# Kernel optimization log

Hardware: AMD Instinct MI355X
Metric: run time of the kernel (lower is better)

The kernel has to match this reference:

```python
import jax, jax.numpy as jnp
import numpy as np

N, C, K2 = 40000, 128, 9  # active voxels, channels, 3x3 kernel taps
HEAD_OUT = {"hm": 3, "center": 2, "center_z": 1, "dim": 3, "rot": 2}
EPS = 1e-5
INIT_BIAS = -2.66


def setup_inputs() -> dict:
    key = jax.random.key(0)
    ks = jax.random.split(key, 16)
    feats = jax.random.normal(ks[0], (N, C), dtype=jnp.float32)
    # precomputed submanifold-conv neighbor indices (one per kernel tap, all valid)
    nbr_idx = jax.random.randint(ks[1], (N, K2), 0, N, dtype=jnp.int32)
    H = len(HEAD_OUT)
    inp = {"feats": feats, "nbr_idx": nbr_idx}
    # stacked 3x3 SubMConv weights for all heads (kaiming-ish scale)
    inp["W1"] = jax.random.normal(ks[2], (H, K2, C, C), dtype=jnp.float32) * (2.0 / (K2 * C)) ** 0.5
    inp["gamma"] = jnp.ones((H, C), jnp.float32)
    inp["beta"] = jnp.zeros((H, C), jnp.float32)
    for i, (name, oc) in enumerate(HEAD_OUT.items()):
        inp[f"w_{name}"] = jax.random.normal(ks[3 + i], (C, oc), dtype=jnp.float32) * (2.0 / C) ** 0.5
        inp[f"b_{name}"] = (jnp.full((oc,), INIT_BIAS, jnp.float32) if name == "hm"
                             else jnp.zeros((oc,), jnp.float32))
    return inp


def reference(feats, nbr_idx, W1, gamma, beta,
              w_hm, b_hm, w_center, b_center, w_center_z, b_center_z,
              w_dim, b_dim, w_rot, b_rot):
    # SubMConv2d as gather + contraction over kernel taps (shared by all heads)
    gathered = feats[nbr_idx]                       # [N, K2, C]
    y = jnp.einsum('nkc,hkcd->hnd', gathered, W1)   # [H, N, C]
    # BatchNorm1d (training-mode forward: biased batch stats over voxels) + ReLU
    mean = y.mean(axis=1, keepdims=True)
    var = y.var(axis=1, keepdims=True)
    y = jax.nn.relu((y - mean) * jax.lax.rsqrt(var + EPS) * gamma[:, None, :] + beta[:, None, :])
    # per-head 1x1 SubMConv with bias
    heads = [(w_hm, b_hm), (w_center, b_center), (w_center_z, b_center_z),
             (w_dim, b_dim), (w_rot, b_rot)]
    outs = [y[i] @ w + b for i, (w, b) in enumerate(heads)]
    # concat head outputs along channel: [N, 3+2+1+3+2] = [N, 11]
    return jnp.concatenate(outs, axis=-1)
```

## Files before the change

kernel.cpp:

```cpp
#include <hip/hip_runtime.h>
#include <stdint.h>

#define NVOX 40000
#define CCH  128
#define K2   9
#define NH   5

typedef __attribute__((ext_vector_type(8))) short bf16x8;
typedef __attribute__((ext_vector_type(4))) float f32x4;

__device__ __forceinline__ unsigned short f2b(float f) {
  union { float f; unsigned int u; } v; v.f = f;
  return (unsigned short)((v.u + 0x7fffu + ((v.u >> 16) & 1u)) >> 16);
}
__device__ __forceinline__ float b2f(unsigned short u) {
  union { unsigned int u; float f; } v; v.u = ((unsigned int)u) << 16;
  return v.f;
}
__device__ __forceinline__ void g2l16(const void* g, void* l) {
  __builtin_amdgcn_global_load_lds(
      (const __attribute__((address_space(1))) unsigned int*)g,
      (__attribute__((address_space(3))) unsigned int*)l, 16, 0, 0);
}
__device__ __forceinline__ int swz(int row, int col) {
  return row * 128 + ((((col >> 3) ^ (row & 15)) << 3) | (col & 7));
}

__global__ void cvt_feats(const float4* __restrict__ in, ushort4* __restrict__ o, int n4) {
  int i = blockIdx.x * 256 + threadIdx.x;
  if (i < n4) {
    float4 v = in[i];
    ushort4 r;
    r.x = f2b(v.x); r.y = f2b(v.y); r.z = f2b(v.z); r.w = f2b(v.w);
    o[i] = r;
  }
}

__global__ void cvt_w1(const float* __restrict__ w1, unsigned short* __restrict__ w1t) {
  __shared__ unsigned short t[128 * 34];
  int tile = blockIdx.x;
  int q = blockIdx.y;
  const float* src = w1 + (size_t)tile * 16384 + q * 32 * 128;
  for (int e = threadIdx.x; e < 4096; e += 256) {
    int c = e >> 7, d = e & 127;
    t[d * 34 + c] = f2b(src[e]);
  }
  __syncthreads();
  unsigned short* dst = w1t + (size_t)tile * 16384 + q * 32;
  for (int e = threadIdx.x; e < 4096; e += 256) {
    int d = e >> 5, c = e & 31;
    dst[d * 128 + c] = t[d * 34 + c];
  }
}

__global__ void __launch_bounds__(256, 2) conv_gemm(
    const unsigned short* __restrict__ fb,
    const int* __restrict__ nbr,
    const unsigned short* __restrict__ w1t,
    unsigned short* __restrict__ yb,
    float* __restrict__ sums)
{
  __shared__ unsigned short As[128 * 128];
  __shared__ unsigned short Bs[128 * 128];
  __shared__ int idxs[128 * K2];

  const int h = blockIdx.y;
  const int n0 = blockIdx.x * 128;
  const int tid = threadIdx.x;
  const int wave = tid >> 6;
  const int lane = tid & 63;
  const int lrow = lane >> 4;
  const int lcol = lane & 15;
  const int wm = wave >> 1, wn = wave & 1;

  for (int i = tid; i < 128 * K2; i += 256) {
    int r = i / K2;
    int kk = i - r * K2;
    int gn = n0 + r; if (gn > NVOX - 1) gn = NVOX - 1;
    idxs[i] = nbr[gn * K2 + kk];
  }
  __syncthreads();

  f32x4 acc[4][4] = {};

  for (int k = 0; k < K2; ++k) {
    const unsigned short* wp = w1t + (((size_t)h * K2 + k) << 14);
#pragma unroll
    for (int i = 0; i < 8; ++i) {
      int elem = wave * 4096 + i * 512;
      int row = (elem >> 7) + lrow;
      g2l16(wp + row * 128 + ((lcol ^ (row & 15)) << 3), &Bs[elem]);
    }
    int ridx[8];
#pragma unroll
    for (int i = 0; i < 8; ++i)
      ridx[i] = idxs[(wave * 32 + i * 4 + lrow) * K2 + k];
#pragma unroll
    for (int i = 0; i < 8; ++i) {
      int row = wave * 32 + i * 4 + lrow;
      g2l16(fb + (size_t)ridx[i] * CCH + ((lcol ^ (row & 15)) << 3),
            &As[(wave * 32 + i * 4) * CCH]);
    }

    __syncthreads();
#pragma unroll
    for (int kc = 0; kc < 4; ++kc) {
      bf16x8 af[4], bfr[4];
#pragma unroll
      for (int mi = 0; mi < 4; ++mi) {
        int row = wm * 64 + mi * 16 + lcol;
        af[mi] = *(const bf16x8*)&As[row * CCH + (((kc * 4 + lrow) ^ (row & 15)) << 3)];
      }
#pragma unroll
      for (int ni = 0; ni < 4; ++ni) {
        int row = wn * 64 + ni * 16 + lcol;
        bfr[ni] = *(const bf16x8*)&Bs[row * CCH + (((kc * 4 + lrow) ^ (row & 15)) << 3)];
      }
#pragma unroll
      for (int mi = 0; mi < 4; ++mi)
#pragma unroll
        for (int ni = 0; ni < 4; ++ni)
          acc[mi][ni] = __builtin_amdgcn_mfma_f32_16x16x32_bf16(af[mi], bfr[ni], acc[mi][ni], 0, 0, 0);
    }
    __syncthreads();
  }

#pragma unroll
  for (int mi = 0; mi < 4; ++mi)
#pragma unroll
    for (int ni = 0; ni < 4; ++ni)
#pragma unroll
      for (int r = 0; r < 4; ++r) {
        int row = wm * 64 + mi * 16 + lrow * 4 + r;
        int col = wn * 64 + ni * 16 + lcol;
        As[swz(row, col)] = f2b(acc[mi][ni][r]);
      }
  __syncthreads();

  for (int i = tid; i < 2048; i += 256) {
    int row = i >> 4;
    int c = i & 15;
    if (n0 + row < NVOX)
      *(bf16x8*)(yb + ((size_t)h * NVOX + n0 + row) * CCH + c * 8) =
          *(const bf16x8*)&As[row * 128 + ((c ^ (row & 15)) << 3)];
  }

  {
    int col = tid & 127, half = tid >> 7;
    int rbase = half * 64;
    int nvalid = NVOX - n0 - rbase;
    if (nvalid > 64) nvalid = 64;
    float s = 0.f, q = 0.f;
    for (int r = 0; r < nvalid; ++r) {
      float z = b2f(As[swz(rbase + r, col)]);
      s += z; q += z * z;
    }
    if (nvalid > 0) {
      atomicAdd(&sums[h * CCH + col], s);
      atomicAdd(&sums[NH * CCH + h * CCH + col], q);
    }
  }
}

__global__ void finalize_bn(const float* __restrict__ sums, const float* __restrict__ gamma,
                            const float* __restrict__ beta, float* __restrict__ ssb) {
  int h = blockIdx.x, c = threadIdx.x;
  float mean = sums[h * CCH + c] * (1.f / NVOX);
  float var = sums[NH * CCH + h * CCH + c] * (1.f / NVOX) - mean * mean;
  float rstd = rsqrtf(var + 1e-5f);
  float scale = rstd * gamma[h * CCH + c];
  ssb[h * CCH + c] = scale;
  ssb[NH * CCH + h * CCH + c] = beta[h * CCH + c] - mean * scale;
}

__global__ void __launch_bounds__(256) head_fuse(
    const unsigned short* __restrict__ yb, const float* __restrict__ ssb,
    const float* __restrict__ w_hm, const float* __restrict__ b_hm,
    const float* __restrict__ w_ce, const float* __restrict__ b_ce,
    const float* __restrict__ w_cz, const float* __restrict__ b_cz,
    const float* __restrict__ w_dm, const float* __restrict__ b_dm,
    const float* __restrict__ w_rt, const float* __restrict__ b_rt,
    float* __restrict__ out)
{
  int v = blockIdx.x * 256 + threadIdx.x;
  if (v >= NVOX) return;
  float a0 = b_hm[0], a1 = b_hm[1], a2 = b_hm[2];
  float a3 = b_ce[0], a4 = b_ce[1];
  float a5 = b_cz[0];
  float a6 = b_dm[0], a7 = b_dm[1], a8 = b_dm[2];
  float a9 = b_rt[0], a10 = b_rt[1];

#define DO_HEAD(HI, BODY)                                                    \
  {                                                                          \
    const bf16x8* yp = (const bf16x8*)(yb + ((size_t)(HI)*NVOX + v) * CCH);  \
    const float* sc = ssb + (HI)*CCH;                                        \
    const float* sh = ssb + NH * CCH + (HI)*CCH;                             \
    for (int q8 = 0; q8 < 16; ++q8) {                                        \
      bf16x8 pk = yp[q8];                                                    \
      _Pragma("unroll") for (int e = 0; e < 8; ++e) {                        \
        int d = q8 * 8 + e;                                                  \
        float z = fmaf(b2f((unsigned short)pk[e]), sc[d], sh[d]);            \
        z = fmaxf(z, 0.f);                                                   \
        BODY;                                                                \
      }                                                                      \
    }                                                                        \
  }

  DO_HEAD(0, { a0 = fmaf(z, w_hm[d*3+0], a0); a1 = fmaf(z, w_hm[d*3+1], a1); a2 = fmaf(z, w_hm[d*3+2], a2); })
  DO_HEAD(1, { a3 = fmaf(z, w_ce[d*2+0], a3); a4 = fmaf(z, w_ce[d*2+1], a4); })
  DO_HEAD(2, { a5 = fmaf(z, w_cz[d], a5); })
  DO_HEAD(3, { a6 = fmaf(z, w_dm[d*3+0], a6); a7 = fmaf(z, w_dm[d*3+1], a7); a8 = fmaf(z, w_dm[d*3+2], a8); })
  DO_HEAD(4, { a9 = fmaf(z, w_rt[d*2+0], a9); a10 = fmaf(z, w_rt[d*2+1], a10); })
#undef DO_HEAD

  float* op = out + (size_t)v * 11;
  op[0] = a0; op[1] = a1; op[2] = a2; op[3] = a3; op[4] = a4; op[5] = a5;
  op[6] = a6; op[7] = a7; op[8] = a8; op[9] = a9; op[10] = a10;
}

extern "C" void kernel_launch(void* const* d_in, const int* in_sizes, int n_in,
                              void* d_out, int out_size, void* d_ws, size_t ws_size,
                              hipStream_t stream) {
  const float* feats = (const float*)d_in[0];
  const int*   nbr   = (const int*)d_in[1];
  const float* W1    = (const float*)d_in[2];
  const float* gamma = (const float*)d_in[3];
  const float* beta  = (const float*)d_in[4];
  const float* w_hm = (const float*)d_in[5];  const float* b_hm = (const float*)d_in[6];
  const float* w_ce = (const float*)d_in[7];  const float* b_ce = (const float*)d_in[8];
  const float* w_cz = (const float*)d_in[9];  const float* b_cz = (const float*)d_in[10];
  const float* w_dm = (const float*)d_in[11]; const float* b_dm = (const float*)d_in[12];
  const float* w_rt = (const float*)d_in[13]; const float* b_rt = (const float*)d_in[14];
  float* out = (float*)d_out;

  char* ws = (char*)d_ws;
  unsigned short* w1t = (unsigned short*)ws;
  unsigned short* fb  = (unsigned short*)(ws + 11796480);
  unsigned short* yb  = (unsigned short*)(ws + 22036480);
  float* sums = (float*)(ws + 73236480);
  float* ssb  = (float*)(ws + 73241600);

  hipMemsetAsync(sums, 0, 2 * NH * CCH * sizeof(float), stream);
  cvt_feats<<<5000, 256, 0, stream>>>((const float4*)feats, (ushort4*)fb, NVOX * CCH / 4);
  cvt_w1<<<dim3(45, 4), 256, 0, stream>>>(W1, w1t);
  conv_gemm<<<dim3(313, NH), 256, 0, stream>>>(fb, nbr, w1t, yb, sums);
  finalize_bn<<<NH, CCH, 0, stream>>>(sums, gamma, beta, ssb);
  head_fuse<<<157, 256, 0, stream>>>(yb, ssb, w_hm, b_hm, w_ce, b_ce, w_cz, b_cz,
                                     w_dm, b_dm, w_rt, b_rt, out);
}
```

Measured before the change: 244.2 us.

## Read conv weights from global, prefetch gathers, regroup blocks, split head kernel

The conv GEMM no longer stages weights in LDS. Each wave reads its B fragments directly from global memory, which frees LDS and lets occupancy rise to 3 blocks per SM. The next tap's feature gather is issued after the MFMA loop, and blocks are reordered so the 5 heads of each group of 8 tiles run close together to share gathered rows in cache. The two conversion kernels are merged into one launch, and the head kernel now uses one thread per (head, voxel) for more parallelism. The risk is that uncached global B loads and the single-buffered As add latency and can stall the MFMAs.

```diff
diff --git a/kernel.cpp b/kernel.cpp
--- a/kernel.cpp
+++ b/kernel.cpp
@@ -5,6 +5,7 @@
 #define CCH  128
 #define K2   9
 #define NH   5
+#define TILES 313
 
 typedef __attribute__((ext_vector_type(8))) short bf16x8;
 typedef __attribute__((ext_vector_type(4))) float f32x4;
@@ -26,20 +27,23 @@
   return row * 128 + ((((col >> 3) ^ (row & 15)) << 3) | (col & 7));
 }
 
-__global__ void cvt_feats(const float4* __restrict__ in, ushort4* __restrict__ o, int n4) {
-  int i = blockIdx.x * 256 + threadIdx.x;
-  if (i < n4) {
-    float4 v = in[i];
-    ushort4 r;
-    r.x = f2b(v.x); r.y = f2b(v.y); r.z = f2b(v.z); r.w = f2b(v.w);
-    o[i] = r;
-  }
-}
-
-__global__ void cvt_w1(const float* __restrict__ w1, unsigned short* __restrict__ w1t) {
+__global__ void prep(const float4* __restrict__ feats, ushort4* __restrict__ fb,
+                     const float* __restrict__ w1, unsigned short* __restrict__ w1t) {
   __shared__ unsigned short t[128 * 34];
-  int tile = blockIdx.x;
-  int q = blockIdx.y;
+  int b = blockIdx.x;
+  if (b < 5000) {
+    int i = b * 256 + threadIdx.x;
+    if (i < NVOX * CCH / 4) {
+      float4 v = feats[i];
+      ushort4 r;
+      r.x = f2b(v.x); r.y = f2b(v.y); r.z = f2b(v.z); r.w = f2b(v.w);
+      fb[i] = r;
+    }
+    return;
+  }
+  int bb = b - 5000;
+  int tile = bb >> 2;
+  int q = bb & 3;
   const float* src = w1 + (size_t)tile * 16384 + q * 32 * 128;
   for (int e = threadIdx.x; e < 4096; e += 256) {
     int c = e >> 7, d = e & 127;
@@ -53,7 +57,7 @@
   }
 }
 
-__global__ void __launch_bounds__(256, 2) conv_gemm(
+__global__ void __launch_bounds__(256, 3) conv_gemm(
     const unsigned short* __restrict__ fb,
     const int* __restrict__ nbr,
     const unsigned short* __restrict__ w1t,
@@ -61,11 +65,17 @@
     float* __restrict__ sums)
 {
   __shared__ unsigned short As[128 * 128];
-  __shared__ unsigned short Bs[128 * 128];
   __shared__ int idxs[128 * K2];
 
-  const int h = blockIdx.y;
-  const int n0 = blockIdx.x * 128;
+  const int bid = blockIdx.x;
+  const int s = bid / 40;
+  const int r = bid % 40;
+  const int h = r >> 3;
+  const int x = r & 7;
+  const int tile = s * 8 + x;
+  if (tile >= TILES) return;
+  const int n0 = tile * 128;
+
   const int tid = threadIdx.x;
   const int wave = tid >> 6;
   const int lane = tid & 63;
@@ -74,55 +84,65 @@
   const int wm = wave >> 1, wn = wave & 1;
 
   for (int i = tid; i < 128 * K2; i += 256) {
-    int r = i / K2;
-    int kk = i - r * K2;
-    int gn = n0 + r; if (gn > NVOX - 1) gn = NVOX - 1;
+    int rr = i / K2;
+    int kk = i - rr * K2;
+    int gn = n0 + rr; if (gn > NVOX - 1) gn = NVOX - 1;
     idxs[i] = nbr[gn * K2 + kk];
   }
   __syncthreads();
 
   f32x4 acc[4][4] = {};
 
-  for (int k = 0; k < K2; ++k) {
-    const unsigned short* wp = w1t + (((size_t)h * K2 + k) << 14);
-#pragma unroll
-    for (int i = 0; i < 8; ++i) {
-      int elem = wave * 4096 + i * 512;
-      int row = (elem >> 7) + lrow;
-      g2l16(wp + row * 128 + ((lcol ^ (row & 15)) << 3), &Bs[elem]);
-    }
+  {
     int ridx[8];
 #pragma unroll
     for (int i = 0; i < 8; ++i)
-      ridx[i] = idxs[(wave * 32 + i * 4 + lrow) * K2 + k];
+      ridx[i] = idxs[(wave * 32 + i * 4 + lrow) * K2 + 0];
 #pragma unroll
     for (int i = 0; i < 8; ++i) {
       int row = wave * 32 + i * 4 + lrow;
       g2l16(fb + (size_t)ridx[i] * CCH + ((lcol ^ (row & 15)) << 3),
             &As[(wave * 32 + i * 4) * CCH]);
     }
-
+  }
+
+  for (int k = 0; k < K2; ++k) {
+    const unsigned short* wp = w1t + (((size_t)h * K2 + k) << 14);
     __syncthreads();
+
 #pragma unroll
     for (int kc = 0; kc < 4; ++kc) {
       bf16x8 af[4], bfr[4];
+#pragma unroll
+      for (int ni = 0; ni < 4; ++ni) {
+        int row = wn * 64 + ni * 16 + lcol;
+        bfr[ni] = *(const bf16x8*)(wp + row * CCH + kc * 32 + lrow * 8);
+      }
 #pragma unroll
       for (int mi = 0; mi < 4; ++mi) {
         int row = wm * 64 + mi * 16 + lcol;
         af[mi] = *(const bf16x8*)&As[row * CCH + (((kc * 4 + lrow) ^ (row & 15)) << 3)];
       }
 #pragma unroll
-      for (int ni = 0; ni < 4; ++ni) {
-        int row = wn * 64 + ni * 16 + lcol;
-        bfr[ni] = *(const bf16x8*)&Bs[row * CCH + (((kc * 4 + lrow) ^ (row & 15)) << 3)];
-      }
-#pragma unroll
       for (int mi = 0; mi < 4; ++mi)
 #pragma unroll
         for (int ni = 0; ni < 4; ++ni)
           acc[mi][ni] = __builtin_amdgcn_mfma_f32_16x16x32_bf16(af[mi], bfr[ni], acc[mi][ni], 0, 0, 0);
     }
     __syncthreads();
+
+    if (k + 1 < K2) {
+      int ridx[8];
+#pragma unroll
+      for (int i = 0; i < 8; ++i)
+        ridx[i] = idxs[(wave * 32 + i * 4 + lrow) * K2 + k + 1];
+#pragma unroll
+      for (int i = 0; i < 8; ++i) {
+        int row = wave * 32 + i * 4 + lrow;
+        g2l16(fb + (size_t)ridx[i] * CCH + ((lcol ^ (row & 15)) << 3),
+              &As[(wave * 32 + i * 4) * CCH]);
+      }
+    }
   }
 
 #pragma unroll
@@ -130,10 +150,10 @@
 #pragma unroll
     for (int ni = 0; ni < 4; ++ni)
 #pragma unroll
-      for (int r = 0; r < 4; ++r) {
-        int row = wm * 64 + mi * 16 + lrow * 4 + r;
+      for (int rr = 0; rr < 4; ++rr) {
+        int row = wm * 64 + mi * 16 + lrow * 4 + rr;
         int col = wn * 64 + ni * 16 + lcol;
-        As[swz(row, col)] = f2b(acc[mi][ni][r]);
+        As[swz(row, col)] = f2b(acc[mi][ni][rr]);
       }
   __syncthreads();
 
@@ -150,13 +170,13 @@
     int rbase = half * 64;
     int nvalid = NVOX - n0 - rbase;
     if (nvalid > 64) nvalid = 64;
-    float s = 0.f, q = 0.f;
-    for (int r = 0; r < nvalid; ++r) {
-      float z = b2f(As[swz(rbase + r, col)]);
-      s += z; q += z * z;
+    float sm = 0.f, q = 0.f;
+    for (int rr = 0; rr < nvalid; ++rr) {
+      float z = b2f(As[swz(rbase + rr, col)]);
+      sm += z; q += z * z;
     }
     if (nvalid > 0) {
-      atomicAdd(&sums[h * CCH + col], s);
+      atomicAdd(&sums[h * CCH + col], sm);
       atomicAdd(&sums[NH * CCH + h * CCH + col], q);
     }
   }
@@ -182,40 +202,44 @@
     const float* __restrict__ w_rt, const float* __restrict__ b_rt,
     float* __restrict__ out)
 {
-  int v = blockIdx.x * 256 + threadIdx.x;
-  if (v >= NVOX) return;
-  float a0 = b_hm[0], a1 = b_hm[1], a2 = b_hm[2];
-  float a3 = b_ce[0], a4 = b_ce[1];
-  float a5 = b_cz[0];
-  float a6 = b_dm[0], a7 = b_dm[1], a8 = b_dm[2];
-  float a9 = b_rt[0], a10 = b_rt[1];
-
-#define DO_HEAD(HI, BODY)                                                    \
-  {                                                                          \
-    const bf16x8* yp = (const bf16x8*)(yb + ((size_t)(HI)*NVOX + v) * CCH);  \
-    const float* sc = ssb + (HI)*CCH;                                        \
-    const float* sh = ssb + NH * CCH + (HI)*CCH;                             \
-    for (int q8 = 0; q8 < 16; ++q8) {                                        \
-      bf16x8 pk = yp[q8];                                                    \
-      _Pragma("unroll") for (int e = 0; e < 8; ++e) {                        \
-        int d = q8 * 8 + e;                                                  \
-        float z = fmaf(b2f((unsigned short)pk[e]), sc[d], sh[d]);            \
-        z = fmaxf(z, 0.f);                                                   \
-        BODY;                                                                \
-      }                                                                      \
-    }                                                                        \
-  }
-
-  DO_HEAD(0, { a0 = fmaf(z, w_hm[d*3+0], a0); a1 = fmaf(z, w_hm[d*3+1], a1); a2 = fmaf(z, w_hm[d*3+2], a2); })
-  DO_HEAD(1, { a3 = fmaf(z, w_ce[d*2+0], a3); a4 = fmaf(z, w_ce[d*2+1], a4); })
-  DO_HEAD(2, { a5 = fmaf(z, w_cz[d], a5); })
-  DO_HEAD(3, { a6 = fmaf(z, w_dm[d*3+0], a6); a7 = fmaf(z, w_dm[d*3+1], a7); a8 = fmaf(z, w_dm[d*3+2], a8); })
-  DO_HEAD(4, { a9 = fmaf(z, w_rt[d*2+0], a9); a10 = fmaf(z, w_rt[d*2+1], a10); })
-#undef DO_HEAD
-
-  float* op = out + (size_t)v * 11;
-  op[0] = a0; op[1] = a1; op[2] = a2; op[3] = a3; op[4] = a4; op[5] = a5;
-  op[6] = a6; op[7] = a7; op[8] = a8; op[9] = a9; op[10] = a10;
+  int t = blockIdx.x * 256 + threadIdx.x;
+  if (t >= NH * NVOX) return;
+  int h = t / NVOX;
+  int v = t - h * NVOX;
+
+  const float* wp; const float* bp; int oc, off;
+  switch (h) {
+    case 0: wp = w_hm; bp = b_hm; oc = 3; off = 0; break;
+    case 1: wp = w_ce; bp = b_ce; oc = 2; off = 3; break;
+    case 2: wp = w_cz; bp = b_cz; oc = 1; off = 5; break;
+    case 3: wp = w_dm; bp = b_dm; oc = 3; off = 6; break;
+    default: wp = w_rt; bp = b_rt; oc = 2; off = 9; break;
+  }
+  float a0 = bp[0];
+  float a1 = (oc > 1) ? bp[1] : 0.f;
+  float a2 = (oc > 2) ? bp[2] : 0.f;
+
+  const bf16x8* yp = (const bf16x8*)(yb + ((size_t)h * NVOX + v) * CCH);
+  const float* sc = ssb + h * CCH;
+  const float* sh = ssb + NH * CCH + h * CCH;
+
+  for (int q8 = 0; q8 < 16; ++q8) {
+    bf16x8 pk = yp[q8];
+#pragma unroll
+    for (int e = 0; e < 8; ++e) {
+      int d = q8 * 8 + e;
+      float z = fmaf(b2f((unsigned short)pk[e]), sc[d], sh[d]);
+      z = fmaxf(z, 0.f);
+      const float* wr = wp + d * oc;
+      a0 = fmaf(z, wr[0], a0);
+      if (oc > 1) a1 = fmaf(z, wr[1], a1);
+      if (oc > 2) a2 = fmaf(z, wr[2], a2);
+    }
+  }
+  float* op = out + (size_t)v * 11 + off;
+  op[0] = a0;
+  if (oc > 1) op[1] = a1;
+  if (oc > 2) op[2] = a2;
 }
 
 extern "C" void kernel_launch(void* const* d_in, const int* in_sizes, int n_in,
@@ -241,10 +265,9 @@
   float* ssb  = (float*)(ws + 73241600);
 
   hipMemsetAsync(sums, 0, 2 * NH * CCH * sizeof(float), stream);
-  cvt_feats<<<5000, 256, 0, stream>>>((const float4*)feats, (ushort4*)fb, NVOX * CCH / 4);
-  cvt_w1<<<dim3(45, 4), 256, 0, stream>>>(W1, w1t);
-  conv_gemm<<<dim3(313, NH), 256, 0, stream>>>(fb, nbr, w1t, yb, sums);
+  prep<<<5180, 256, 0, stream>>>((const float4*)feats, (ushort4*)fb, W1, w1t);
+  conv_gemm<<<1600, 256, 0, stream>>>(fb, nbr, w1t, yb, sums);
   finalize_bn<<<NH, CCH, 0, stream>>>(sums, gamma, beta, ssb);
-  head_fuse<<<157, 256, 0, stream>>>(yb, ssb, w_hm, b_hm, w_ce, b_ce, w_cz, b_cz,
+  head_fuse<<<782, 256, 0, stream>>>(yb, ssb, w_hm, b_hm, w_ce, b_ce, w_cz, b_cz,
                                      w_dm, b_dm, w_rt, b_rt, out);
 }
```

New measurement: 286.3 us. +17.3%, slower.
